# Kernel tuning notes

Measured on AMD Instinct MI355X. Metric: run time of the kernel, lower is better.

The kernel has to match this reference:

```python
import jax, jax.numpy as jnp
import numpy as np
from jax import lax

# 4D convolution: XLA's general conv supports 4 spatial dims directly.
# dim numbers: N C + 4 spatial (H1 W1 H2 W2)
_DN = ('NCHWDT', 'OIHWDT', 'NCHWDT')


def conv4d(x, w, b):
    # x: [B, Cin, H1, W1, H2, W2]; w: [Cout, Cin, 3,3,3,3]; b: [Cout]
    y = lax.conv_general_dilated(x, w, window_strides=(1, 1, 1, 1),
                                 padding=[(1, 1)] * 4,
                                 dimension_numbers=_DN)
    return y + b.reshape(1, -1, 1, 1, 1, 1)


def setup_inputs() -> dict:
    key = jax.random.key(0)
    ks = jax.random.split(key, 7)
    B, S = 2, 30
    x = jax.random.normal(ks[0], (B, 1, S, S, S, S), dtype=jnp.float32)
    # Conv4d weights, fan-in scaled (kernel 3^4 = 81)
    w1 = jax.random.normal(ks[1], (10, 1, 3, 3, 3, 3), dtype=jnp.float32) * (1.0 / np.sqrt(1 * 81))
    b1 = jax.random.normal(ks[2], (10,), dtype=jnp.float32) * 0.01
    w2 = jax.random.normal(ks[3], (10, 10, 3, 3, 3, 3), dtype=jnp.float32) * (1.0 / np.sqrt(10 * 81))
    b2 = jax.random.normal(ks[4], (10,), dtype=jnp.float32) * 0.01
    w3 = jax.random.normal(ks[5], (1, 10, 3, 3, 3, 3), dtype=jnp.float32) * (1.0 / np.sqrt(10 * 81))
    b3 = jax.random.normal(ks[6], (1,), dtype=jnp.float32) * 0.01
    return {"x": x, "w1": w1, "b1": b1, "w2": w2, "b2": b2, "w3": w3, "b3": b3}


def reference(x, w1, b1, w2, b2, w3, b3):
    def net(t):
        for w, b in ((w1, b1), (w2, b2), (w3, b3)):
            t = jax.nn.relu(conv4d(t, w, b))
        return t

    # symmetric mode: f(x) + permute(f(permute(x)))
    perm = (0, 1, 4, 5, 2, 3)
    return net(x) + jnp.transpose(net(jnp.transpose(x, perm)), perm)
```

## Files before the change

kernel.cpp:

```cpp
#include <hip/hip_runtime.h>


static constexpr int S  = 30;
static constexpr long S4 = 810000;
static constexpr size_t PLANE = 32768;
static constexpr size_t YBYTES = (size_t)1800 * PLANE;

typedef __bf16 bf16x8 __attribute__((ext_vector_type(8)));
typedef float  f32x16 __attribute__((ext_vector_type(16)));
typedef unsigned int  u32;
typedef unsigned short u16;

static __device__ __forceinline__ u16 f2bf(float f) {
    u32 u = __builtin_bit_cast(u32, f);
    return (u16)((u + 0x7fffu + ((u >> 16) & 1u)) >> 16);
}

__global__ __launch_bounds__(256) void prep_k(u32* __restrict__ ft,
    const float* __restrict__ w1, const float* __restrict__ w2,
    const float* __restrict__ w3, u16* __restrict__ y1, u16* __restrict__ y2)
{
    const int tid = threadIdx.x;
    if (blockIdx.x >= 42) {
        const int pb = blockIdx.x - 42;
        if (tid >= 124) return;
        int hp, tp;
        if (tid < 32)      { hp = 0;        tp = tid; }
        else if (tid < 64) { hp = 31;       tp = tid - 32; }
        else if (tid < 94) { hp = tid - 63; tp = 0; }
        else               { hp = tid - 93; tp = 31; }
        const size_t off = (size_t)pb * PLANE + hp * 1024 + tp * 32;
        const uint4 z = make_uint4(0, 0, 0, 0);
        *(uint4*)((char*)y1 + off)      = z;
        *(uint4*)((char*)y1 + off + 16) = z;
        *(uint4*)((char*)y2 + off)      = z;
        *(uint4*)((char*)y2 + off + 16) = z;
        return;
    }
    const int gid = blockIdx.x * 256 + tid;
    const int lane = gid & 63;
    const int n = lane & 31, hl = lane >> 5;
    u16 us[8];
#pragma unroll
    for (int j = 0; j < 8; ++j) us[j] = 0;

    if (gid < 6 * 27 * 64) {
        int r = gid >> 6;
        const int k3 = r % 3; r /= 3;
        const int k12 = r % 9; const int set = r / 9;
        const int layer = set >> 1, swap = set & 1;
        const int k1 = k12 / 3, k2 = k12 % 3;
        if (n < 30) {
            const int k4 = (n < 10) ? 0 : ((n < 20) ? 1 : 2);
            const int co = n - 10 * k4;
            const int i1 = swap ? k3 : k1, i2 = swap ? k4 : k2;
            const int i3 = swap ? k1 : k3, i4 = swap ? k2 : k4;
            const int widx = ((i1 * 3 + i2) * 3 + i3) * 3 + i4;
#pragma unroll
            for (int j = 0; j < 8; ++j) {
                const int k = hl * 8 + j;
                float wv = 0.f;
                if (layer == 0) { if (k == 0) wv = w1[co * 81 + widx]; }
                else if (layer == 1) { if (k < 10) wv = w2[(co * 10 + k) * 81 + widx]; }
                else { if (k < 10 && co == 0) wv = w3[k * 81 + widx]; }
                us[j] = f2bf(wv);
            }
        }
    } else {
        const int idx = gid - 6 * 27 * 64;
        int r = idx >> 6;
        const int k3 = r % 3, swap = r / 3;
        if (n < 30) {
            const int k4 = (n < 10) ? 0 : ((n < 20) ? 1 : 2);
            const int co = n - 10 * k4;
#pragma unroll
            for (int j = 0; j < 8; ++j) {
                const int k12 = hl * 8 + j;
                if (k12 < 9) {
                    const int k1 = k12 / 3, k2 = k12 % 3;
                    const int i1 = swap ? k3 : k1, i2 = swap ? k4 : k2;
                    const int i3 = swap ? k1 : k3, i4 = swap ? k2 : k4;
                    const int widx = ((i1 * 3 + i2) * 3 + i3) * 3 + i4;
                    us[j] = f2bf(w1[co * 81 + widx]);
                }
            }
        }
    }
    u32* o = ft + (size_t)gid * 4;
    o[0] = (u32)us[0] | ((u32)us[1] << 16);
    o[1] = (u32)us[2] | ((u32)us[3] << 16);
    o[2] = (u32)us[4] | ((u32)us[5] << 16);
    o[3] = (u32)us[6] | ((u32)us[7] << 16);
}

__global__ __launch_bounds__(256, 4) void conv0_k(
    const float* __restrict__ x, const uint4* __restrict__ bt,
    const float* __restrict__ bias, void* __restrict__ outp)
{
    __shared__ float E[4][1056];
    const int wgid = blockIdx.x + S * blockIdx.y + 900 * blockIdx.z;
    const int id2  = (wgid & 7) * 450 + (wgid >> 3);
    const int half = id2 & 1;
    int sp = id2 >> 1;
    const int w1i = sp % S; sp /= S;
    const int h1  = sp % S;
    const int b   = sp / S;

    const int tid = threadIdx.x;
    const int lane = tid & 63, wv = tid >> 6;
    const int m = lane & 31, hl = lane >> 5;
    const int rbase = half * 15 + wv * 4;

    uint4 Bs[3];
#pragma unroll
    for (int ss = 0; ss < 3; ++ss) Bs[ss] = bt[ss * 64 + lane];

    int gof[9]; int gokm = 0;
#pragma unroll
    for (int k12 = 0; k12 < 9; ++k12) {
        const int g1 = h1 + k12 / 3 - 1, g2 = w1i + k12 % 3 - 1;
        gof[k12] = 0;
        if (g1 >= 0 && g1 < S && g2 >= 0 && g2 < S) {
            gof[k12] = (g1 * S + g2) * 900; gokm |= 1 << k12;
        }
    }
    const float* xb = x + (size_t)b * S4;

    uint4 F[6];
#pragma unroll
    for (int f = 0; f < 6; ++f) {
        const int hp = rbase + f;
        const bool rk = (hp >= 1 && hp <= 30 && m >= 1 && m <= 30);
        const int ro = (hp - 1) * 30 + (m - 1);
        u16 av[8];
#pragma unroll
        for (int j = 0; j < 8; ++j) av[j] = 0;
        if (hl == 0) {
#pragma unroll
            for (int j = 0; j < 8; ++j) {
                float v = 0.f;
                if (rk && ((gokm >> j) & 1)) v = xb[gof[j] + ro];
                av[j] = f2bf(v);
            }
        } else {
            float v = 0.f;
            if (rk && ((gokm >> 8) & 1)) v = xb[gof[8] + ro];
            av[0] = f2bf(v);
        }
        F[f] = make_uint4((u32)av[0] | ((u32)av[1] << 16),
                          (u32)av[2] | ((u32)av[3] << 16),
                          (u32)av[4] | ((u32)av[5] << 16),
                          (u32)av[6] | ((u32)av[7] << 16));
    }

    f32x16 acc[4];
#pragma unroll
    for (int r = 0; r < 4; ++r)
#pragma unroll
        for (int e = 0; e < 16; ++e) acc[r][e] = 0.f;
#pragma unroll
    for (int ss = 0; ss < 3; ++ss)
#pragma unroll
        for (int r = 0; r < 4; ++r)
            acc[r] = __builtin_amdgcn_mfma_f32_32x32x16_bf16(
                __builtin_bit_cast(bf16x8, F[r + ss]),
                __builtin_bit_cast(bf16x8, Bs[ss]), acc[r], 0, 0, 0);

    float* Ew = E[wv];
    for (int r = 0; r < 4; ++r) {
        if (wv == 3 && r == 3) continue;
#pragma unroll
        for (int gq = 0; gq < 4; ++gq)
#pragma unroll
            for (int r4 = 0; r4 < 4; ++r4)
                Ew[m * 33 + 4 * hl + 8 * gq + r4] = acc[r][gq * 4 + r4];

        const int h2 = rbase + r;
        char* pl = (char*)outp + ((size_t)b * 900 + h1 * S + w1i) * PLANE
                   + (size_t)(h2 + 1) * 1024;
        const int t = lane >> 1, h8 = lane & 1;
        if (t < 30) {
            u32 wo[4];
#pragma unroll
            for (int p = 0; p < 4; ++p) {
                const int c0 = 8 * h8 + 2 * p, c1 = c0 + 1;
                float v0 = 0.f, v1 = 0.f;
                if (c0 < 10)
                    v0 = fmaxf(Ew[c0 * 33 + t] + Ew[(10 + c0) * 33 + t + 1]
                             + Ew[(20 + c0) * 33 + t + 2] + bias[c0], 0.f);
                if (c1 < 10)
                    v1 = fmaxf(Ew[c1 * 33 + t] + Ew[(10 + c1) * 33 + t + 1]
                             + Ew[(20 + c1) * 33 + t + 2] + bias[c1], 0.f);
                wo[p] = (u32)f2bf(v0) | ((u32)f2bf(v1) << 16);
            }
            *(uint4*)(pl + (t + 1) * 32 + h8 * 16) =
                make_uint4(wo[0], wo[1], wo[2], wo[3]);
        }
    }
}

template<int LAYER, bool ACCUM>
__global__ __launch_bounds__(256, 2) void conv_k(
    const void* __restrict__ inp, const u32* __restrict__ ftab,
    const float* __restrict__ bias, void* __restrict__ outp)
{
    __shared__ float E[4][1056];
    __shared__ uint4 BT[1728];

    const int tid = threadIdx.x;
    {
        const uint4* g = (const uint4*)ftab;
#pragma unroll
        for (int j = 0; j < 7; ++j) {
            const int idx = j * 256 + tid;
            if (idx < 1728) BT[idx] = g[idx];
        }
    }
    __syncthreads();

    const int wgid = blockIdx.x + S * blockIdx.y + 900 * blockIdx.z;
    const int id2  = (wgid & 7) * 450 + (wgid >> 3);
    const int half = id2 & 1;
    int sp = id2 >> 1;
    const int w1i = sp % S; sp /= S;
    const int h1  = sp % S;
    const int b   = sp / S;

    const int lane = tid & 63, wv = tid >> 6;
    const int m = lane & 31, hl = lane >> 5;
    const int rbase = half * 15 + wv * 4;

    int rofs[6];
#pragma unroll
    for (int f = 0; f < 6; ++f) {
        int rr = rbase + f; if (rr > 31) rr = 31;
        rofs[f] = rr * 1024;
    }

    int kl[9], nk = 0;
#pragma unroll
    for (int k12 = 0; k12 < 9; ++k12) {
        const int g1 = h1 + k12 / 3 - 1, g2 = w1i + k12 % 3 - 1;
        if (g1 >= 0 && g1 < S && g2 >= 0 && g2 < S)
            kl[nk++] = (g1 * S + g2) | (k12 << 10);
    }

    f32x16 acc[4];
#pragma unroll
    for (int r = 0; r < 4; ++r)
#pragma unroll
        for (int e = 0; e < 16; ++e) acc[r][e] = 0.f;

    auto loadA = [&](uint4* Fd, int g) {
        const char* P = (const char*)inp + ((size_t)b * 900 + g) * PLANE
                        + m * 32 + hl * 16;
#pragma unroll
        for (int f = 0; f < 6; ++f)
            Fd[f] = *(const uint4*)(P + rofs[f]);
    };

    uint4 B0[3];
    {
        const int k0 = kl[0] >> 10;
#pragma unroll
        for (int f = 0; f < 3; ++f) B0[f] = BT[(k0 * 3 + f) * 64 + lane];
    }
    uint4 F[6];
    loadA(F, kl[0] & 1023);

    for (int ki = 0; ki + 1 < nk; ++ki) {
        const int gn = kl[ki + 1] & 1023, kn = kl[ki + 1] >> 10;
        uint4 FN[6];
        loadA(FN, gn);
        uint4 BN[3];
#pragma unroll
        for (int f = 0; f < 3; ++f) BN[f] = BT[(kn * 3 + f) * 64 + lane];

#pragma unroll
        for (int ss = 0; ss < 3; ++ss)
#pragma unroll
            for (int r = 0; r < 4; ++r)
                acc[r] = __builtin_amdgcn_mfma_f32_32x32x16_bf16(
                    __builtin_bit_cast(bf16x8, F[r + ss]),
                    __builtin_bit_cast(bf16x8, B0[ss]), acc[r], 0, 0, 0);

#pragma unroll
        for (int f = 0; f < 6; ++f) F[f] = FN[f];
#pragma unroll
        for (int f = 0; f < 3; ++f) B0[f] = BN[f];
    }
#pragma unroll
    for (int ss = 0; ss < 3; ++ss)
#pragma unroll
        for (int r = 0; r < 4; ++r)
            acc[r] = __builtin_amdgcn_mfma_f32_32x32x16_bf16(
                __builtin_bit_cast(bf16x8, F[r + ss]),
                __builtin_bit_cast(bf16x8, B0[ss]), acc[r], 0, 0, 0);

    float* Ew = E[wv];
    for (int r = 0; r < 4; ++r) {
        if (wv == 3 && r == 3) continue;
#pragma unroll
        for (int gq = 0; gq < 4; ++gq)
#pragma unroll
            for (int r4 = 0; r4 < 4; ++r4)
                Ew[m * 33 + 4 * hl + 8 * gq + r4] = acc[r][gq * 4 + r4];

        const int h2 = rbase + r;
        if (LAYER <= 1) {
            char* pl = (char*)outp + ((size_t)b * 900 + h1 * S + w1i) * PLANE
                       + (size_t)(h2 + 1) * 1024;
            const int t = lane >> 1, h8 = lane & 1;
            if (t < 30) {
                u32 wo[4];
#pragma unroll
                for (int p = 0; p < 4; ++p) {
                    const int c0 = 8 * h8 + 2 * p, c1 = c0 + 1;
                    float v0 = 0.f, v1 = 0.f;
                    if (c0 < 10)
                        v0 = fmaxf(Ew[c0 * 33 + t] + Ew[(10 + c0) * 33 + t + 1]
                                 + Ew[(20 + c0) * 33 + t + 2] + bias[c0], 0.f);
                    if (c1 < 10)
                        v1 = fmaxf(Ew[c1 * 33 + t] + Ew[(10 + c1) * 33 + t + 1]
                                 + Ew[(20 + c1) * 33 + t + 2] + bias[c1], 0.f);
                    wo[p] = (u32)f2bf(v0) | ((u32)f2bf(v1) << 16);
                }
                *(uint4*)(pl + (t + 1) * 32 + h8 * 16) =
                    make_uint4(wo[0], wo[1], wo[2], wo[3]);
            }
        } else {
            if (lane < 30) {
                const int t = lane;
                float v = Ew[t] + Ew[330 + t + 1] + Ew[660 + t + 2] + bias[0];
                v = fmaxf(v, 0.f);
                float* o = (float*)outp + (size_t)b * S4
                           + (size_t)(h1 * S + w1i) * 900 + h2 * 30 + t;
                if (ACCUM) *o += v; else *o = v;
            }
        }
    }
}

extern "C" void kernel_launch(void* const* d_in, const int* in_sizes, int n_in,
                              void* d_out, int out_size, void* d_ws, size_t ws_size,
                              hipStream_t stream)
{
    const float* x   = (const float*)d_in[0];
    const float* w1p = (const float*)d_in[1];
    const float* b1p = (const float*)d_in[2];
    const float* w2p = (const float*)d_in[3];
    const float* b2p = (const float*)d_in[4];
    const float* w3p = (const float*)d_in[5];
    const float* b3p = (const float*)d_in[6];
    float* out = (float*)d_out;

    u32* ft = (u32*)d_ws;
    const uint4* ftL0 = (const uint4*)d_ws + 6 * 27 * 64;
    u16* y1 = (u16*)((char*)d_ws + 172032);
    u16* y2 = (u16*)((char*)y1 + YBYTES);

    prep_k<<<1842, 256, 0, stream>>>(ft, w1p, w2p, w3p, y1, y2);

    dim3 grid(S, S, 4), blk(256);
    for (int br = 0; br < 2; ++br) {
        const u32* f2 = ft + (size_t)(2 + br) * 27 * 64 * 4;
        const u32* f3 = ft + (size_t)(4 + br) * 27 * 64 * 4;
        conv0_k<<<grid, blk, 0, stream>>>(x, ftL0 + br * 192, b1p, (void*)y1);
        conv_k<1, false><<<grid, blk, 0, stream>>>(y1, f2, b2p, (void*)y2);
        if (br == 0)
            conv_k<2, false><<<grid, blk, 0, stream>>>(y2, f3, b3p, (void*)out);
        else
            conv_k<2, true><<<grid, blk, 0, stream>>>(y2, f3, b3p, (void*)out);
    }
}
```

Measured before the change: 384.1 us.

## Fuse both symmetric branches in first and last conv layers

The first layer now computes both branch outputs (original and permuted weights) from a single gather of input fragments, writing into two separate buffers. The last layer processes both branches in one kernel and sums them directly into the output, which removes the read-modify-write accumulate pass. Two kernel launches go away, along with duplicated input loads. The cost is a third workspace buffer (with a fallback path if workspace is too small), plus more LDS and register pressure in the fused kernels.

```diff
diff --git a/kernel.cpp b/kernel.cpp
--- a/kernel.cpp
+++ b/kernel.cpp
@@ -18,7 +18,8 @@
 
 __global__ __launch_bounds__(256) void prep_k(u32* __restrict__ ft,
     const float* __restrict__ w1, const float* __restrict__ w2,
-    const float* __restrict__ w3, u16* __restrict__ y1, u16* __restrict__ y2)
+    const float* __restrict__ w3, u16* __restrict__ p1,
+    u16* __restrict__ p2, u16* __restrict__ p3)
 {
     const int tid = threadIdx.x;
     if (blockIdx.x >= 42) {
@@ -31,10 +32,12 @@
         else               { hp = tid - 93; tp = 31; }
         const size_t off = (size_t)pb * PLANE + hp * 1024 + tp * 32;
         const uint4 z = make_uint4(0, 0, 0, 0);
-        *(uint4*)((char*)y1 + off)      = z;
-        *(uint4*)((char*)y1 + off + 16) = z;
-        *(uint4*)((char*)y2 + off)      = z;
-        *(uint4*)((char*)y2 + off + 16) = z;
+        *(uint4*)((char*)p1 + off)      = z;
+        *(uint4*)((char*)p1 + off + 16) = z;
+        *(uint4*)((char*)p2 + off)      = z;
+        *(uint4*)((char*)p2 + off + 16) = z;
+        *(uint4*)((char*)p3 + off)      = z;
+        *(uint4*)((char*)p3 + off + 16) = z;
         return;
     }
     const int gid = blockIdx.x * 256 + tid;
@@ -93,28 +96,10 @@
     o[3] = (u32)us[6] | ((u32)us[7] << 16);
 }
 
-__global__ __launch_bounds__(256, 4) void conv0_k(
-    const float* __restrict__ x, const uint4* __restrict__ bt,
-    const float* __restrict__ bias, void* __restrict__ outp)
-{
-    __shared__ float E[4][1056];
-    const int wgid = blockIdx.x + S * blockIdx.y + 900 * blockIdx.z;
-    const int id2  = (wgid & 7) * 450 + (wgid >> 3);
-    const int half = id2 & 1;
-    int sp = id2 >> 1;
-    const int w1i = sp % S; sp /= S;
-    const int h1  = sp % S;
-    const int b   = sp / S;
-
-    const int tid = threadIdx.x;
-    const int lane = tid & 63, wv = tid >> 6;
-    const int m = lane & 31, hl = lane >> 5;
-    const int rbase = half * 15 + wv * 4;
-
-    uint4 Bs[3];
-#pragma unroll
-    for (int ss = 0; ss < 3; ++ss) Bs[ss] = bt[ss * 64 + lane];
-
+static __device__ __forceinline__ void l0_frags(
+    const float* __restrict__ x, int b, int h1, int w1i, int rbase,
+    int m, int hl, uint4* F)
+{
     int gof[9]; int gokm = 0;
 #pragma unroll
     for (int k12 = 0; k12 < 9; ++k12) {
@@ -125,8 +110,6 @@
         }
     }
     const float* xb = x + (size_t)b * S4;
-
-    uint4 F[6];
 #pragma unroll
     for (int f = 0; f < 6; ++f) {
         const int hp = rbase + f;
@@ -152,21 +135,13 @@
                           (u32)av[4] | ((u32)av[5] << 16),
                           (u32)av[6] | ((u32)av[7] << 16));
     }
-
-    f32x16 acc[4];
-#pragma unroll
-    for (int r = 0; r < 4; ++r)
-#pragma unroll
-        for (int e = 0; e < 16; ++e) acc[r][e] = 0.f;
-#pragma unroll
-    for (int ss = 0; ss < 3; ++ss)
-#pragma unroll
-        for (int r = 0; r < 4; ++r)
-            acc[r] = __builtin_amdgcn_mfma_f32_32x32x16_bf16(
-                __builtin_bit_cast(bf16x8, F[r + ss]),
-                __builtin_bit_cast(bf16x8, Bs[ss]), acc[r], 0, 0, 0);
-
-    float* Ew = E[wv];
+}
+
+static __device__ __forceinline__ void plane_epilogue(
+    float* Ew, const f32x16* acc, const float* __restrict__ bias,
+    void* __restrict__ outp, int b, int h1, int w1i, int rbase,
+    int m, int hl, int lane, int wv)
+{
     for (int r = 0; r < 4; ++r) {
         if (wv == 3 && r == 3) continue;
 #pragma unroll
@@ -196,6 +171,104 @@
             *(uint4*)(pl + (t + 1) * 32 + h8 * 16) =
                 make_uint4(wo[0], wo[1], wo[2], wo[3]);
         }
+    }
+}
+
+__global__ __launch_bounds__(256, 4) void conv0_k(
+    const float* __restrict__ x, const uint4* __restrict__ bt,
+    const float* __restrict__ bias, void* __restrict__ outp)
+{
+    __shared__ float E[4][1056];
+    const int wgid = blockIdx.x + S * blockIdx.y + 900 * blockIdx.z;
+    const int id2  = (wgid & 7) * 450 + (wgid >> 3);
+    const int half = id2 & 1;
+    int sp = id2 >> 1;
+    const int w1i = sp % S; sp /= S;
+    const int h1  = sp % S;
+    const int b   = sp / S;
+    const int tid = threadIdx.x;
+    const int lane = tid & 63, wv = tid >> 6;
+    const int m = lane & 31, hl = lane >> 5;
+    const int rbase = half * 15 + wv * 4;
+
+    uint4 Bs[3];
+#pragma unroll
+    for (int ss = 0; ss < 3; ++ss) Bs[ss] = bt[ss * 64 + lane];
+
+    uint4 F[6];
+    l0_frags(x, b, h1, w1i, rbase, m, hl, F);
+
+    f32x16 acc[4];
+#pragma unroll
+    for (int r = 0; r < 4; ++r)
+#pragma unroll
+        for (int e = 0; e < 16; ++e) acc[r][e] = 0.f;
+#pragma unroll
+    for (int ss = 0; ss < 3; ++ss)
+#pragma unroll
+        for (int r = 0; r < 4; ++r)
+            acc[r] = __builtin_amdgcn_mfma_f32_32x32x16_bf16(
+                __builtin_bit_cast(bf16x8, F[r + ss]),
+                __builtin_bit_cast(bf16x8, Bs[ss]), acc[r], 0, 0, 0);
+
+    plane_epilogue(E[wv], acc, bias, outp, b, h1, w1i, rbase, m, hl, lane, wv);
+}
+
+__global__ __launch_bounds__(256, 2) void conv0ab_k(
+    const float* __restrict__ x, const uint4* __restrict__ bt,
+    const float* __restrict__ bias, void* __restrict__ y1a,
+    void* __restrict__ y1b)
+{
+    __shared__ float E[4][1056];
+    const int wgid = blockIdx.x + S * blockIdx.y + 900 * blockIdx.z;
+    const int id2  = (wgid & 7) * 450 + (wgid >> 3);
+    const int half = id2 & 1;
+    int sp = id2 >> 1;
+    const int w1i = sp % S; sp /= S;
+    const int h1  = sp % S;
+    const int b   = sp / S;
+    const int tid = threadIdx.x;
+    const int lane = tid & 63, wv = tid >> 6;
+    const int m = lane & 31, hl = lane >> 5;
+    const int rbase = half * 15 + wv * 4;
+
+    uint4 F[6];
+    l0_frags(x, b, h1, w1i, rbase, m, hl, F);
+
+    f32x16 acc[4];
+    {
+        uint4 Bs[3];
+#pragma unroll
+        for (int ss = 0; ss < 3; ++ss) Bs[ss] = bt[ss * 64 + lane];
+#pragma unroll
+        for (int r = 0; r < 4; ++r)
+#pragma unroll
+            for (int e = 0; e < 16; ++e) acc[r][e] = 0.f;
+#pragma unroll
+        for (int ss = 0; ss < 3; ++ss)
+#pragma unroll
+            for (int r = 0; r < 4; ++r)
+                acc[r] = __builtin_amdgcn_mfma_f32_32x32x16_bf16(
+                    __builtin_bit_cast(bf16x8, F[r + ss]),
+                    __builtin_bit_cast(bf16x8, Bs[ss]), acc[r], 0, 0, 0);
+        plane_epilogue(E[wv], acc, bias, y1a, b, h1, w1i, rbase, m, hl, lane, wv);
+    }
+    {
+        uint4 Bs[3];
+#pragma unroll
+        for (int ss = 0; ss < 3; ++ss) Bs[ss] = bt[192 + ss * 64 + lane];
+#pragma unroll
+        for (int r = 0; r < 4; ++r)
+#pragma unroll
+            for (int e = 0; e < 16; ++e) acc[r][e] = 0.f;
+#pragma unroll
+        for (int ss = 0; ss < 3; ++ss)
+#pragma unroll
+            for (int r = 0; r < 4; ++r)
+                acc[r] = __builtin_amdgcn_mfma_f32_32x32x16_bf16(
+                    __builtin_bit_cast(bf16x8, F[r + ss]),
+                    __builtin_bit_cast(bf16x8, Bs[ss]), acc[r], 0, 0, 0);
+        plane_epilogue(E[wv], acc, bias, y1b, b, h1, w1i, rbase, m, hl, lane, wv);
     }
 }
 
@@ -341,6 +414,138 @@
     }
 }
 
+__global__ __launch_bounds__(256, 2) void conv2ab_k(
+    const void* __restrict__ y2a, const void* __restrict__ y2b,
+    const u32* __restrict__ fta, const u32* __restrict__ ftb,
+    const float* __restrict__ bias, float* __restrict__ out)
+{
+    __shared__ uint4 BTS[2][1728];
+
+    const int tid = threadIdx.x;
+    {
+        const uint4* ga = (const uint4*)fta;
+        const uint4* gb = (const uint4*)ftb;
+#pragma unroll
+        for (int j = 0; j < 7; ++j) {
+            const int idx = j * 256 + tid;
+            if (idx < 1728) { BTS[0][idx] = ga[idx]; BTS[1][idx] = gb[idx]; }
+        }
+    }
+    __syncthreads();
+
+    const int wgid = blockIdx.x + S * blockIdx.y + 900 * blockIdx.z;
+    const int id2  = (wgid & 7) * 450 + (wgid >> 3);
+    const int half = id2 & 1;
+    int sp = id2 >> 1;
+    const int w1i = sp % S; sp /= S;
+    const int h1  = sp % S;
+    const int b   = sp / S;
+
+    const int lane = tid & 63, wv = tid >> 6;
+    const int m = lane & 31, hl = lane >> 5;
+    const int rbase = half * 15 + wv * 4;
+
+    int rofs[6];
+#pragma unroll
+    for (int f = 0; f < 6; ++f) {
+        int rr = rbase + f; if (rr > 31) rr = 31;
+        rofs[f] = rr * 1024;
+    }
+
+    int kl[9], nk = 0;
+#pragma unroll
+    for (int k12 = 0; k12 < 9; ++k12) {
+        const int g1 = h1 + k12 / 3 - 1, g2 = w1i + k12 % 3 - 1;
+        if (g1 >= 0 && g1 < S && g2 >= 0 && g2 < S)
+            kl[nk++] = (g1 * S + g2) | (k12 << 10);
+    }
+
+    f32x16 acc[4];
+
+    auto run_taps = [&](const void* inp, const uint4* BTb) {
+#pragma unroll
+        for (int r = 0; r < 4; ++r)
+#pragma unroll
+            for (int e = 0; e < 16; ++e) acc[r][e] = 0.f;
+        auto loadA = [&](uint4* Fd, int g) {
+            const char* P = (const char*)inp + ((size_t)b * 900 + g) * PLANE
+                            + m * 32 + hl * 16;
+#pragma unroll
+            for (int f = 0; f < 6; ++f)
+                Fd[f] = *(const uint4*)(P + rofs[f]);
+        };
+        uint4 B0[3];
+        {
+            const int k0 = kl[0] >> 10;
+#pragma unroll
+            for (int f = 0; f < 3; ++f) B0[f] = BTb[(k0 * 3 + f) * 64 + lane];
+        }
+        uint4 F[6];
+        loadA(F, kl[0] & 1023);
+        for (int ki = 0; ki + 1 < nk; ++ki) {
+            const int gn = kl[ki + 1] & 1023, kn = kl[ki + 1] >> 10;
+            uint4 FN[6];
+            loadA(FN, gn);
+            uint4 BN[3];
+#pragma unroll
+            for (int f = 0; f < 3; ++f) BN[f] = BTb[(kn * 3 + f) * 64 + lane];
+#pragma unroll
+            for (int ss = 0; ss < 3; ++ss)
+#pragma unroll
+                for (int r = 0; r < 4; ++r)
+                    acc[r] = __builtin_amdgcn_mfma_f32_32x32x16_bf16(
+                        __builtin_bit_cast(bf16x8, F[r + ss]),
+                        __builtin_bit_cast(bf16x8, B0[ss]), acc[r], 0, 0, 0);
+#pragma unroll
+            for (int f = 0; f < 6; ++f) F[f] = FN[f];
+#pragma unroll
+            for (int f = 0; f < 3; ++f) B0[f] = BN[f];
+        }
+#pragma unroll
+        for (int ss = 0; ss < 3; ++ss)
+#pragma unroll
+            for (int r = 0; r < 4; ++r)
+                acc[r] = __builtin_amdgcn_mfma_f32_32x32x16_bf16(
+                    __builtin_bit_cast(bf16x8, F[r + ss]),
+                    __builtin_bit_cast(bf16x8, B0[ss]), acc[r], 0, 0, 0);
+    };
+
+    run_taps(y2a, BTS[0]);
+    __syncthreads();
+    float* Ew = (float*)&BTS[0][0] + wv * 1056;
+
+    float va[4] = {0.f, 0.f, 0.f, 0.f};
+    for (int r = 0; r < 4; ++r) {
+        if (wv == 3 && r == 3) continue;
+#pragma unroll
+        for (int gq = 0; gq < 4; ++gq)
+#pragma unroll
+            for (int r4 = 0; r4 < 4; ++r4)
+                Ew[m * 33 + 4 * hl + 8 * gq + r4] = acc[r][gq * 4 + r4];
+        if (lane < 30) {
+            const int t = lane;
+            va[r] = fmaxf(Ew[t] + Ew[330 + t + 1] + Ew[660 + t + 2] + bias[0], 0.f);
+        }
+    }
+
+    run_taps(y2b, BTS[1]);
+    for (int r = 0; r < 4; ++r) {
+        if (wv == 3 && r == 3) continue;
+#pragma unroll
+        for (int gq = 0; gq < 4; ++gq)
+#pragma unroll
+            for (int r4 = 0; r4 < 4; ++r4)
+                Ew[m * 33 + 4 * hl + 8 * gq + r4] = acc[r][gq * 4 + r4];
+        const int h2 = rbase + r;
+        if (lane < 30) {
+            const int t = lane;
+            float v = fmaxf(Ew[t] + Ew[330 + t + 1] + Ew[660 + t + 2] + bias[0], 0.f);
+            out[(size_t)b * S4 + (size_t)(h1 * S + w1i) * 900 + h2 * 30 + t]
+                = va[r] + v;
+        }
+    }
+}
+
 extern "C" void kernel_launch(void* const* d_in, const int* in_sizes, int n_in,
                               void* d_out, int out_size, void* d_ws, size_t ws_size,
                               hipStream_t stream)
@@ -356,20 +561,38 @@
 
     u32* ft = (u32*)d_ws;
     const uint4* ftL0 = (const uint4*)d_ws + 6 * 27 * 64;
-    u16* y1 = (u16*)((char*)d_ws + 172032);
-    u16* y2 = (u16*)((char*)y1 + YBYTES);
-
-    prep_k<<<1842, 256, 0, stream>>>(ft, w1p, w2p, w3p, y1, y2);
+    u16* y1a = (u16*)((char*)d_ws + 172032);
+    u16* y1b = (u16*)((char*)y1a + YBYTES);
+    u16* y2a = (u16*)((char*)y1b + YBYTES);
+
+    const u32* f2b0 = ft + (size_t)2 * 27 * 64 * 4;
+    const u32* f2b1 = ft + (size_t)3 * 27 * 64 * 4;
+    const u32* f3b0 = ft + (size_t)4 * 27 * 64 * 4;
+    const u32* f3b1 = ft + (size_t)5 * 27 * 64 * 4;
 
     dim3 grid(S, S, 4), blk(256);
-    for (int br = 0; br < 2; ++br) {
-        const u32* f2 = ft + (size_t)(2 + br) * 27 * 64 * 4;
-        const u32* f3 = ft + (size_t)(4 + br) * 27 * 64 * 4;
-        conv0_k<<<grid, blk, 0, stream>>>(x, ftL0 + br * 192, b1p, (void*)y1);
-        conv_k<1, false><<<grid, blk, 0, stream>>>(y1, f2, b2p, (void*)y2);
-        if (br == 0)
-            conv_k<2, false><<<grid, blk, 0, stream>>>(y2, f3, b3p, (void*)out);
-        else
-            conv_k<2, true><<<grid, blk, 0, stream>>>(y2, f3, b3p, (void*)out);
-    }
-}
+    const size_t need = 172032 + 3 * YBYTES;
+
+    if (ws_size >= need) {
+        u16* y2b = y1a;
+        prep_k<<<1842, blk, 0, stream>>>(ft, w1p, w2p, w3p, y1a, y1b, y2a);
+        conv0ab_k<<<grid, blk, 0, stream>>>(x, ftL0, b1p, (void*)y1a, (void*)y1b);
+        conv_k<1, false><<<grid, blk, 0, stream>>>(y1a, f2b0, b2p, (void*)y2a);
+        conv_k<1, false><<<grid, blk, 0, stream>>>(y1b, f2b1, b2p, (void*)y2b);
+        conv2ab_k<<<grid, blk, 0, stream>>>(y2a, y2b, f3b0, f3b1, b3p, out);
+    } else {
+        u16* y1 = y1a;
+        u16* y2 = y1b;
+        prep_k<<<1842, blk, 0, stream>>>(ft, w1p, w2p, w3p, y1, y2, y2);
+        for (int br = 0; br < 2; ++br) {
+            const u32* f2 = (br == 0) ? f2b0 : f2b1;
+            const u32* f3 = (br == 0) ? f3b0 : f3b1;
+            conv0_k<<<grid, blk, 0, stream>>>(x, ftL0 + br * 192, b1p, (void*)y1);
+            conv_k<1, false><<<grid, blk, 0, stream>>>(y1, f2, b2p, (void*)y2);
+            if (br == 0)
+                conv_k<2, false><<<grid, blk, 0, stream>>>(y2, f3, b3p, (void*)out);
+            else
+                conv_k<2, true><<<grid, blk, 0, stream>>>(y2, f3, b3p, (void*)out);
+        }
+    }
+}
```

New measurement: 375.0 us. -2.4%, faster.
